# Optimization experiments

Hardware: AMD Instinct MI355X
Metric: run time of the kernel (lower is better)

Reference implementation:

```python
import jax, jax.numpy as jnp
import numpy as np

D = 512
H = 8
HD = D // H
SCALE = float(np.sqrt(HD))
LN_EPS = 1e-5


def setup_inputs() -> dict:
    key = jax.random.key(0)
    ks = jax.random.split(key, 10)
    glorot = lambda k: jax.random.uniform(k, (D, D), jnp.float32, -1.0, 1.0) * np.sqrt(6.0 / (D + D))
    return {
        "x": jax.random.normal(ks[0], (4, 2048, D), jnp.float32),
        "Wq": glorot(ks[1]), "bq": jnp.zeros((D,), jnp.float32),
        "Wk": glorot(ks[2]), "bk": jnp.zeros((D,), jnp.float32),
        "Wv": glorot(ks[3]), "bv": jnp.zeros((D,), jnp.float32),
        "Wo": glorot(ks[4]), "bo": jnp.zeros((D,), jnp.float32),
        "ln_gamma": jnp.ones((D,), jnp.float32),
        "ln_beta": jnp.zeros((D,), jnp.float32),
    }


def reference(x, Wq, bq, Wk, bk, Wv, bv, Wo, bo, ln_gamma, ln_beta):
    B, S, _ = x.shape
    # Linear projections (torch Linear: y = x @ W.T + b)
    q = (x @ Wq.T + bq).reshape(B, S, H, HD).transpose(0, 2, 1, 3)  # [B,H,S,HD]
    k = (x @ Wk.T + bk).reshape(B, S, H, HD).transpose(0, 2, 1, 3)
    v = (x @ Wv.T + bv).reshape(B, S, H, HD).transpose(0, 2, 1, 3)
    scores = jnp.einsum('bhqd,bhkd->bhqk', q, k) / SCALE
    attn = jax.nn.softmax(scores, axis=-1)  # dropout is identity in eval mode
    context = jnp.einsum('bhqk,bhkd->bhqd', attn, v)
    context = context.transpose(0, 2, 1, 3).reshape(B, S, D)
    out = context @ Wo.T + bo
    y = x + out  # residual
    mean = jnp.mean(y, axis=-1, keepdims=True)
    var = jnp.var(y, axis=-1, keepdims=True)
    return (y - mean) / jnp.sqrt(var + LN_EPS) * ln_gamma + ln_beta
```

## Files before the change

### kernel.cpp

```cpp
#include <hip/hip_runtime.h>
#include <hip/hip_bf16.h>

#define B_ 4
#define S_ 2048
#define D_ 512
#define H_ 8
#define HD_ 64
#define M_TOT 8192

typedef __attribute__((ext_vector_type(8))) short short8;
typedef __attribute__((ext_vector_type(4))) float f32x4;
typedef __attribute__((ext_vector_type(16))) float f32x16;
typedef unsigned short u16;
typedef unsigned int u32;
typedef unsigned long long u64;

__device__ __forceinline__ u16 f2bf(float f) {
  union { float f; u32 u; } v; v.f = f;
  u32 u = v.u;
  return (u16)((u + 0x7fffu + ((u >> 16) & 1u)) >> 16);
}

__device__ __forceinline__ u32 cvtpk(float lo, float hi) {
  u32 r;
  asm("v_cvt_pk_bf16_f32 %0, %1, %2" : "=v"(r) : "v"(lo), "v"(hi));
  return r;
}

__device__ __forceinline__ float exp2_hw(float x) { return __builtin_amdgcn_exp2f(x); }

__device__ __forceinline__ void gload16(const void* g, void* l) {
  __builtin_amdgcn_global_load_lds(
      (const __attribute__((address_space(1))) unsigned int*)g,
      (__attribute__((address_space(3))) unsigned int*)l, 16, 0, 0);
}

__global__ __launch_bounds__(256) void cast_kernel(
    const float* __restrict__ x, const float* __restrict__ wq, const float* __restrict__ wk,
    const float* __restrict__ wv, const float* __restrict__ wo,
    u16* __restrict__ xb, u16* __restrict__ wqb, u16* __restrict__ wkb,
    u16* __restrict__ wvb, u16* __restrict__ wob)
{
  const int NX = M_TOT * D_ / 4;
  const int NW = D_ * D_ / 4;
  int i = blockIdx.x * 256 + threadIdx.x;
  const float* src; u16* dst; int o;
  if (i < NX)               { src = x;  dst = xb;  o = i; }
  else if (i < NX + NW)     { src = wq; dst = wqb; o = i - NX; }
  else if (i < NX + 2 * NW) { src = wk; dst = wkb; o = i - NX - NW; }
  else if (i < NX + 3 * NW) { src = wv; dst = wvb; o = i - NX - 2 * NW; }
  else if (i < NX + 4 * NW) { src = wo; dst = wob; o = i - NX - 3 * NW; }
  else return;
  f32x4 v = ((const f32x4*)src)[o];
  u32 p0 = (u32)f2bf(v[0]) | ((u32)f2bf(v[1]) << 16);
  u32 p1 = (u32)f2bf(v[2]) | ((u32)f2bf(v[3]) << 16);
  u32* d = (u32*)(dst + (long)o * 4);
  d[0] = p0; d[1] = p1;
}

#define BM 128
#define BN 128
#define BKK 64

__global__ __launch_bounds__(256) void gemm_bt(
    const u16* __restrict__ A, const u16* __restrict__ Bw,
    const float* __restrict__ b0, const float* __restrict__ b1, const float* __restrict__ b2,
    const float* __restrict__ resid,
    u16* __restrict__ oq, u16* __restrict__ ok, u16* __restrict__ ov,
    float* __restrict__ out_f32, float qscale, int mode)
{
  __shared__ u16 As[BM * BKK];
  __shared__ u16 Bs[BN * BKK];
  const int K = D_;
  const int tid = threadIdx.x;
  const int lane = tid & 63;
  const int wave = tid >> 6;
  const int wr = wave >> 1, wc = wave & 1;
  const int m0 = blockIdx.x * BM, n0 = blockIdx.y * BN;
  const int l15 = lane & 15, l4 = lane >> 4;

  f32x4 acc[4][4];
#pragma unroll
  for (int i = 0; i < 4; ++i)
#pragma unroll
    for (int j = 0; j < 4; ++j)
      acc[i][j] = (f32x4){0.f, 0.f, 0.f, 0.f};

  const int srow_in_grp = lane >> 3;
  const int schunk = (lane & 7) * 16;
  const int ssw = srow_in_grp << 4;
  const char* Ab = (const char*)(A + (long)m0 * K);
  const char* Bb = (const char*)(Bw + (long)n0 * K);

  for (int k0 = 0; k0 < K; k0 += BKK) {
    __syncthreads();
#pragma unroll
    for (int i = 0; i < 4; ++i) {
      int row = (wave * 4 + i) * 8 + srow_in_grp;
      long gsrc = (long)row * (K * 2) + k0 * 2 + (schunk ^ ssw);
      gload16(Ab + gsrc, (char*)As + (wave * 4 + i) * 1024);
      gload16(Bb + gsrc, (char*)Bs + (wave * 4 + i) * 1024);
    }
    __syncthreads();

#pragma unroll
    for (int kb = 0; kb < 2; ++kb) {
      short8 af[4], bf[4];
      const int cb = kb * 64 + l4 * 16;
#pragma unroll
      for (int i = 0; i < 4; ++i) {
        int ra = wr * 64 + i * 16 + l15;
        int rb = wc * 64 + i * 16 + l15;
        af[i] = *(const short8*)((const char*)As + ra * 128 + (cb ^ ((ra & 7) << 4)));
        bf[i] = *(const short8*)((const char*)Bs + rb * 128 + (cb ^ ((rb & 7) << 4)));
      }
#pragma unroll
      for (int i = 0; i < 4; ++i)
#pragma unroll
        for (int j = 0; j < 4; ++j)
          acc[i][j] = __builtin_amdgcn_mfma_f32_16x16x32_bf16(af[i], bf[j], acc[i][j], 0, 0, 0);
    }
  }

  if (mode == 0) {
    const int which = n0 >> 9;
    const float* bias = which == 0 ? b0 : (which == 1 ? b1 : b2);
    const float scale = which == 0 ? qscale : 1.0f;
    u16* outp = which == 0 ? oq : (which == 1 ? ok : ov);
#pragma unroll
    for (int i = 0; i < 4; ++i) {
#pragma unroll
      for (int j = 0; j < 4; ++j) {
        int n = n0 + wc * 64 + j * 16 + l15;
        int nn = n & 511;
        float bv = bias[nn];
        int h = nn >> 6, hd = nn & 63;
        int mbase = m0 + wr * 64 + i * 16 + l4 * 4;
        int b = mbase >> 11, s0 = mbase & 2047;
        if (which == 2) {
          int s0p = (s0 & ~12) | ((s0 & 4) << 1) | ((s0 & 8) >> 1);
          union { u16 u[4]; u64 ll; } pk;
#pragma unroll
          for (int r = 0; r < 4; ++r)
            pk.u[r] = f2bf(acc[i][j][r] + bv);
          *(u64*)&outp[((long)(b * H_ + h) * HD_ + hd) * S_ + s0p] = pk.ll;
        } else {
#pragma unroll
          for (int r = 0; r < 4; ++r) {
            float v = (acc[i][j][r] + bv) * scale;
            outp[((long)(b * H_ + h) * S_ + s0 + r) * HD_ + hd] = f2bf(v);
          }
        }
      }
    }
  } else {
#pragma unroll
    for (int i = 0; i < 4; ++i) {
#pragma unroll
      for (int j = 0; j < 4; ++j) {
        int n = n0 + wc * 64 + j * 16 + l15;
        float bv = b0[n];
#pragma unroll
        for (int r = 0; r < 4; ++r) {
          int m = m0 + wr * 64 + i * 16 + l4 * 4 + r;
          long idx = (long)m * D_ + n;
          out_f32[idx] = acc[i][j][r] + bv + resid[idx];
        }
      }
    }
  }
}

__global__ __launch_bounds__(256) void attn_kernel(
    const u16* __restrict__ Qg, const u16* __restrict__ Kg,
    const u16* __restrict__ Vtg, u16* __restrict__ ctx)
{
  __shared__ char Ks[2][8192];
  __shared__ char Vs[2][8192];

  const int tid = threadIdx.x, lane = tid & 63, wave = tid >> 6;
  const int l31 = lane & 31, lh = lane >> 5;
  const int lin = blockIdx.x;
  const int wg = (lin & 7) * 64 + (lin >> 3);
  const int bh = wg >> 4;
  const int q0 = (wg & 15) * 128;
  const int b = bh >> 3, h = bh & 7;
  const long hoff = (long)bh * S_ * HD_;
  const u16* Qh = Qg + hoff;
  const char* Kb = (const char*)(Kg + hoff);
  const char* Vb = (const char*)(Vtg + hoff);
  const int qw = q0 + wave * 32;

  const int srow = lane >> 3;
  const int soff = ((lane & 7) * 16) ^ (srow << 4);

  short8 qf[4];
#pragma unroll
  for (int dc = 0; dc < 4; ++dc)
    qf[dc] = *(const short8*)&Qh[(long)(qw + l31) * HD_ + dc * 16 + lh * 8];

  float mrun = -1e30f, lrun = 0.f;
  f32x16 oacc[2];
#pragma unroll
  for (int db = 0; db < 2; ++db)
#pragma unroll
    for (int r = 0; r < 16; ++r) oacc[db][r] = 0.f;

#pragma unroll
  for (int j = 0; j < 2; ++j) {
    int r = wave * 16 + j * 8 + srow;
    gload16(Kb + (long)r * 128 + soff, Ks[0] + (wave * 2 + j) * 1024);
    gload16(Vb + (long)r * 4096 + soff, Vs[0] + (wave * 2 + j) * 1024);
  }
  __syncthreads();

  for (int t = 0; t < S_ / 64; ++t) {
    const int cur = t & 1;
    if (t < S_ / 64 - 1) {
      const int kv1 = (t + 1) * 64;
#pragma unroll
      for (int j = 0; j < 2; ++j) {
        int r = wave * 16 + j * 8 + srow;
        gload16(Kb + (long)(kv1 + r) * 128 + soff, Ks[cur ^ 1] + (wave * 2 + j) * 1024);
        gload16(Vb + (long)r * 4096 + (long)kv1 * 2 + soff, Vs[cur ^ 1] + (wave * 2 + j) * 1024);
      }
    }

    f32x16 p0, p1;
    {
      f32x16 a0, a1;
#pragma unroll
      for (int r = 0; r < 16; ++r) { a0[r] = 0.f; a1[r] = 0.f; }
      const int swz = (l31 & 7) << 4;
#pragma unroll
      for (int dc = 0; dc < 4; ++dc) {
        const int cb = dc * 32 + lh * 16;
        short8 k0 = *(const short8*)(Ks[cur] + l31 * 128 + (cb ^ swz));
        short8 k1 = *(const short8*)(Ks[cur] + (32 + l31) * 128 + (cb ^ swz));
        a0 = __builtin_amdgcn_mfma_f32_32x32x16_bf16(k0, qf[dc], a0, 0, 0, 0);
        a1 = __builtin_amdgcn_mfma_f32_32x32x16_bf16(k1, qf[dc], a1, 0, 0, 0);
      }
      p0 = a0; p1 = a1;
    }

    float mt = p0[0];
#pragma unroll
    for (int r = 1; r < 16; ++r) mt = fmaxf(mt, p0[r]);
#pragma unroll
    for (int r = 0; r < 16; ++r) mt = fmaxf(mt, p1[r]);
    mt = fmaxf(mt, __shfl_xor(mt, 32));
    if (__any(mt > mrun + 8.0f)) {
      float mnew = fmaxf(mrun, mt);
      float rs = exp2_hw(mrun - mnew);
      mrun = mnew; lrun *= rs;
#pragma unroll
      for (int db = 0; db < 2; ++db)
#pragma unroll
        for (int r = 0; r < 16; ++r) oacc[db][r] *= rs;
    }
    float sum = 0.f;
#pragma unroll
    for (int r = 0; r < 16; ++r) { float v = exp2_hw(p0[r] - mrun); p0[r] = v; sum += v; }
#pragma unroll
    for (int r = 0; r < 16; ++r) { float v = exp2_hw(p1[r] - mrun); p1[r] = v; sum += v; }
    sum += __shfl_xor(sum, 32);
    lrun += sum;

#pragma unroll
    for (int nt = 0; nt < 2; ++nt) {
#pragma unroll
      for (int ks = 0; ks < 2; ++ks) {
        union { u32 w[4]; short8 s; } pa;
        const f32x16& pp = nt ? p1 : p0;
        pa.w[0] = cvtpk(pp[ks * 8 + 0], pp[ks * 8 + 1]);
        pa.w[1] = cvtpk(pp[ks * 8 + 2], pp[ks * 8 + 3]);
        pa.w[2] = cvtpk(pp[ks * 8 + 4], pp[ks * 8 + 5]);
        pa.w[3] = cvtpk(pp[ks * 8 + 6], pp[ks * 8 + 7]);
        const int colb = nt * 64 + ks * 32 + lh * 16;
#pragma unroll
        for (int db = 0; db < 2; ++db) {
          const int vr = db * 32 + l31;
          short8 vf = *(const short8*)(Vs[cur] + vr * 128 + (colb ^ ((vr & 7) << 4)));
          oacc[db] = __builtin_amdgcn_mfma_f32_32x32x16_bf16(vf, pa.s, oacc[db], 0, 0, 0);
        }
      }
    }

    __syncthreads();
  }

  const float inv = 1.f / lrun;
  u16* crow0 = ctx + (long)(b * S_ + (qw + l31)) * D_ + h * HD_;
#pragma unroll
  for (int db = 0; db < 2; ++db) {
#pragma unroll
    for (int rq = 0; rq < 4; ++rq) {
      const int d0 = db * 32 + rq * 8 + lh * 4;
      u32 lo = cvtpk(oacc[db][rq * 4 + 0] * inv, oacc[db][rq * 4 + 1] * inv);
      u32 hi = cvtpk(oacc[db][rq * 4 + 2] * inv, oacc[db][rq * 4 + 3] * inv);
      *(u64*)(crow0 + d0) = (u64)lo | ((u64)hi << 32);
    }
  }
}

__global__ __launch_bounds__(256) void ln_kernel(
    const float* __restrict__ y, const float* __restrict__ gamma,
    const float* __restrict__ beta, float* __restrict__ out)
{
  const int lane = threadIdx.x & 63, wave = threadIdx.x >> 6;
  const long row = (long)blockIdx.x * 4 + wave;
  const float* yr = y + row * D_;
  f32x4 v0 = *(const f32x4*)&yr[lane * 8];
  f32x4 v1 = *(const f32x4*)&yr[lane * 8 + 4];
  float s = 0.f, ss = 0.f;
#pragma unroll
  for (int e = 0; e < 4; ++e) {
    s += v0[e]; ss += v0[e] * v0[e];
    s += v1[e]; ss += v1[e] * v1[e];
  }
#pragma unroll
  for (int msk = 1; msk < 64; msk <<= 1) {
    s += __shfl_xor(s, msk);
    ss += __shfl_xor(ss, msk);
  }
  float mean = s * (1.f / 512.f);
  float var = ss * (1.f / 512.f) - mean * mean;
  float inv = rsqrtf(var + 1e-5f);
  f32x4 g0 = *(const f32x4*)&gamma[lane * 8];
  f32x4 g1 = *(const f32x4*)&gamma[lane * 8 + 4];
  f32x4 b0 = *(const f32x4*)&beta[lane * 8];
  f32x4 b1 = *(const f32x4*)&beta[lane * 8 + 4];
  f32x4 o0, o1;
#pragma unroll
  for (int e = 0; e < 4; ++e) {
    o0[e] = (v0[e] - mean) * inv * g0[e] + b0[e];
    o1[e] = (v1[e] - mean) * inv * g1[e] + b1[e];
  }
  *(f32x4*)&out[row * D_ + lane * 8] = o0;
  *(f32x4*)&out[row * D_ + lane * 8 + 4] = o1;
}

extern "C" void kernel_launch(void* const* d_in, const int* in_sizes, int n_in,
                              void* d_out, int out_size, void* d_ws, size_t ws_size,
                              hipStream_t stream) {
  const float* x  = (const float*)d_in[0];
  const float* Wq = (const float*)d_in[1];
  const float* bq = (const float*)d_in[2];
  const float* Wk = (const float*)d_in[3];
  const float* bk = (const float*)d_in[4];
  const float* Wv = (const float*)d_in[5];
  const float* bv = (const float*)d_in[6];
  const float* Wo = (const float*)d_in[7];
  const float* bo = (const float*)d_in[8];
  const float* lg = (const float*)d_in[9];
  const float* lb = (const float*)d_in[10];

  char* ws = (char*)d_ws;
  const size_t SZ_XB = (size_t)M_TOT * D_ * 2;
  const size_t SZ_W  = (size_t)D_ * D_ * 2;
  u16* xb   = (u16*)(ws);
  u16* q_ws = (u16*)(ws + SZ_XB);
  u16* k_ws = (u16*)(ws + 2 * SZ_XB);
  u16* vt_ws= (u16*)(ws + 3 * SZ_XB);
  u16* c_ws = (u16*)(ws + 4 * SZ_XB);
  u16* wqb  = (u16*)(ws + 5 * SZ_XB);
  u16* wkb  = (u16*)(ws + 5 * SZ_XB + SZ_W);
  u16* wvb  = (u16*)(ws + 5 * SZ_XB + 2 * SZ_W);
  u16* wob  = (u16*)(ws + 5 * SZ_XB + 3 * SZ_W);
  float* yf = (float*)(ws);

  cast_kernel<<<5120, 256, 0, stream>>>(x, Wq, Wk, Wv, Wo, xb, wqb, wkb, wvb, wob);

  gemm_bt<<<dim3(M_TOT / BM, 1536 / BN), 256, 0, stream>>>(
      xb, wqb, bq, bk, bv, nullptr, q_ws, k_ws, vt_ws, nullptr,
      0.18033688011112042f, 0);

  attn_kernel<<<512, 256, 0, stream>>>(q_ws, k_ws, vt_ws, c_ws);

  gemm_bt<<<dim3(M_TOT / BM, D_ / BN), 256, 0, stream>>>(
      c_ws, wob, bo, nullptr, nullptr, x, nullptr, nullptr, nullptr, yf, 1.0f, 1);

  ln_kernel<<<M_TOT / 4, 256, 0, stream>>>(yf, lg, lb, (float*)d_out);
}
```

Before: 189.3 us.

## Halve attention workgroup size and stage K/V in MFMA-fragment order

```diff
diff --git a/kernel.cpp b/kernel.cpp
--- a/kernel.cpp
+++ b/kernel.cpp
@@ -9,6 +9,7 @@
 #define M_TOT 8192
 
 typedef __attribute__((ext_vector_type(8))) short short8;
+typedef __attribute__((ext_vector_type(2))) float f32x2;
 typedef __attribute__((ext_vector_type(4))) float f32x4;
 typedef __attribute__((ext_vector_type(16))) float f32x16;
 typedef unsigned short u16;
@@ -171,7 +172,7 @@
   }
 }
 
-__global__ __launch_bounds__(256) void attn_kernel(
+__global__ __launch_bounds__(128) void attn_kernel(
     const u16* __restrict__ Qg, const u16* __restrict__ Kg,
     const u16* __restrict__ Vtg, u16* __restrict__ ctx)
 {
@@ -181,9 +182,9 @@
   const int tid = threadIdx.x, lane = tid & 63, wave = tid >> 6;
   const int l31 = lane & 31, lh = lane >> 5;
   const int lin = blockIdx.x;
-  const int wg = (lin & 7) * 64 + (lin >> 3);
-  const int bh = wg >> 4;
-  const int q0 = (wg & 15) * 128;
+  const int wg = (lin & 7) * 128 + (lin >> 3);
+  const int bh = wg >> 5;
+  const int q0 = (wg & 31) * 64;
   const int b = bh >> 3, h = bh & 7;
   const long hoff = (long)bh * S_ * HD_;
   const u16* Qh = Qg + hoff;
@@ -191,8 +192,23 @@
   const char* Vb = (const char*)(Vtg + hoff);
   const int qw = q0 + wave * 32;
 
-  const int srow = lane >> 3;
-  const int soff = ((lane & 7) * 16) ^ (srow << 4);
+  const char* Ksrc = Kb + (long)l31 * 128 + lh * 16;
+  const char* Vsrc = Vb + (long)l31 * 4096 + lh * 16;
+
+#define STAGE(buf, kv0v) do {                                                      \
+    if (wave == 0) {                                                               \
+      _Pragma("unroll") for (int nt = 0; nt < 2; ++nt)                             \
+      _Pragma("unroll") for (int dc = 0; dc < 4; ++dc)                             \
+        gload16(Ksrc + (long)(kv0v) * 128 + nt * 4096 + dc * 32,                   \
+                Ks[buf] + (nt * 4 + dc) * 1024);                                   \
+    } else {                                                                       \
+      _Pragma("unroll") for (int nt = 0; nt < 2; ++nt)                             \
+      _Pragma("unroll") for (int ks = 0; ks < 2; ++ks)                             \
+      _Pragma("unroll") for (int db = 0; db < 2; ++db)                             \
+        gload16(Vsrc + (long)db * 131072 + (kv0v) * 2 + nt * 64 + ks * 32,         \
+                Vs[buf] + ((nt * 2 + ks) * 2 + db) * 1024);                        \
+    }                                                                              \
+  } while (0)
 
   short8 qf[4];
 #pragma unroll
@@ -206,63 +222,53 @@
 #pragma unroll
     for (int r = 0; r < 16; ++r) oacc[db][r] = 0.f;
 
-#pragma unroll
-  for (int j = 0; j < 2; ++j) {
-    int r = wave * 16 + j * 8 + srow;
-    gload16(Kb + (long)r * 128 + soff, Ks[0] + (wave * 2 + j) * 1024);
-    gload16(Vb + (long)r * 4096 + soff, Vs[0] + (wave * 2 + j) * 1024);
-  }
+  STAGE(0, 0);
   __syncthreads();
 
   for (int t = 0; t < S_ / 64; ++t) {
     const int cur = t & 1;
-    if (t < S_ / 64 - 1) {
-      const int kv1 = (t + 1) * 64;
-#pragma unroll
-      for (int j = 0; j < 2; ++j) {
-        int r = wave * 16 + j * 8 + srow;
-        gload16(Kb + (long)(kv1 + r) * 128 + soff, Ks[cur ^ 1] + (wave * 2 + j) * 1024);
-        gload16(Vb + (long)r * 4096 + (long)kv1 * 2 + soff, Vs[cur ^ 1] + (wave * 2 + j) * 1024);
-      }
-    }
+    if (t < S_ / 64 - 1) STAGE(cur ^ 1, (t + 1) * 64);
 
     f32x16 p0, p1;
     {
       f32x16 a0, a1;
 #pragma unroll
       for (int r = 0; r < 16; ++r) { a0[r] = 0.f; a1[r] = 0.f; }
-      const int swz = (l31 & 7) << 4;
 #pragma unroll
       for (int dc = 0; dc < 4; ++dc) {
-        const int cb = dc * 32 + lh * 16;
-        short8 k0 = *(const short8*)(Ks[cur] + l31 * 128 + (cb ^ swz));
-        short8 k1 = *(const short8*)(Ks[cur] + (32 + l31) * 128 + (cb ^ swz));
+        short8 k0 = *(const short8*)(Ks[cur] + (0 * 4 + dc) * 1024 + lane * 16);
+        short8 k1 = *(const short8*)(Ks[cur] + (1 * 4 + dc) * 1024 + lane * 16);
         a0 = __builtin_amdgcn_mfma_f32_32x32x16_bf16(k0, qf[dc], a0, 0, 0, 0);
         a1 = __builtin_amdgcn_mfma_f32_32x32x16_bf16(k1, qf[dc], a1, 0, 0, 0);
       }
       p0 = a0; p1 = a1;
     }
 
-    float mt = p0[0];
-#pragma unroll
-    for (int r = 1; r < 16; ++r) mt = fmaxf(mt, p0[r]);
-#pragma unroll
-    for (int r = 0; r < 16; ++r) mt = fmaxf(mt, p1[r]);
+    const f32x2* v0p = (const f32x2*)&p0;
+    const f32x2* v1p = (const f32x2*)&p1;
+    f32x2 m2 = __builtin_elementwise_max(v0p[0], v1p[0]);
+#pragma unroll
+    for (int r = 1; r < 8; ++r)
+      m2 = __builtin_elementwise_max(m2, __builtin_elementwise_max(v0p[r], v1p[r]));
+    float mt = fmaxf(m2[0], m2[1]);
     mt = fmaxf(mt, __shfl_xor(mt, 32));
     if (__any(mt > mrun + 8.0f)) {
       float mnew = fmaxf(mrun, mt);
       float rs = exp2_hw(mrun - mnew);
       mrun = mnew; lrun *= rs;
-#pragma unroll
-      for (int db = 0; db < 2; ++db)
-#pragma unroll
-        for (int r = 0; r < 16; ++r) oacc[db][r] *= rs;
-    }
-    float sum = 0.f;
-#pragma unroll
-    for (int r = 0; r < 16; ++r) { float v = exp2_hw(p0[r] - mrun); p0[r] = v; sum += v; }
-#pragma unroll
-    for (int r = 0; r < 16; ++r) { float v = exp2_hw(p1[r] - mrun); p1[r] = v; sum += v; }
+      f32x2 rs2 = {rs, rs};
+      f32x2* o2 = (f32x2*)&oacc[0];
+#pragma unroll
+      for (int r = 0; r < 16; ++r) o2[r] *= rs2;
+    }
+#pragma unroll
+    for (int r = 0; r < 16; ++r) p0[r] = exp2_hw(p0[r] - mrun);
+#pragma unroll
+    for (int r = 0; r < 16; ++r) p1[r] = exp2_hw(p1[r] - mrun);
+    f32x2 s2 = v0p[0] + v1p[0];
+#pragma unroll
+    for (int r = 1; r < 8; ++r) s2 += v0p[r] + v1p[r];
+    float sum = s2[0] + s2[1];
     sum += __shfl_xor(sum, 32);
     lrun += sum;
 
@@ -276,11 +282,9 @@
         pa.w[1] = cvtpk(pp[ks * 8 + 2], pp[ks * 8 + 3]);
         pa.w[2] = cvtpk(pp[ks * 8 + 4], pp[ks * 8 + 5]);
         pa.w[3] = cvtpk(pp[ks * 8 + 6], pp[ks * 8 + 7]);
-        const int colb = nt * 64 + ks * 32 + lh * 16;
 #pragma unroll
         for (int db = 0; db < 2; ++db) {
-          const int vr = db * 32 + l31;
-          short8 vf = *(const short8*)(Vs[cur] + vr * 128 + (colb ^ ((vr & 7) << 4)));
+          short8 vf = *(const short8*)(Vs[cur] + ((nt * 2 + ks) * 2 + db) * 1024 + lane * 16);
           oacc[db] = __builtin_amdgcn_mfma_f32_32x32x16_bf16(vf, pa.s, oacc[db], 0, 0, 0);
         }
       }
@@ -301,6 +305,7 @@
       *(u64*)(crow0 + d0) = (u64)lo | ((u64)hi << 32);
     }
   }
+#undef STAGE
 }
 
 __global__ __launch_bounds__(256) void ln_kernel(
@@ -375,7 +380,7 @@
       xb, wqb, bq, bk, bv, nullptr, q_ws, k_ws, vt_ws, nullptr,
       0.18033688011112042f, 0);
 
-  attn_kernel<<<512, 256, 0, stream>>>(q_ws, k_ws, vt_ws, c_ws);
+  attn_kernel<<<1024, 128, 0, stream>>>(q_ws, k_ws, vt_ws, c_ws);
 
   gemm_bt<<<dim3(M_TOT / BM, D_ / BN), 256, 0, stream>>>(
       c_ws, wob, bo, nullptr, nullptr, x, nullptr, nullptr, nullptr, yf, 1.0f, 1);
```

Result: slower. 199.4 us (+5.4%).
